# Optimization experiments

Hardware: AMD Instinct MI355X
Metric: run time of the kernel (lower is better)

## Reference

```python
import jax, jax.numpy as jnp
import numpy as np

POS_HALF = 4   # positive window: [t-4, t+4)
NEG_LEN = 12   # negatives: up to 12 frames on each side of the positive window
K_MAX = 2 * POS_HALF + 2 * NEG_LEN  # 32 candidates max per timestep


def _build_windows(T):
    """Static [T,K_MAX] gather indices + positive/valid masks (numpy, trace-time)."""
    idx = np.zeros((T, K_MAX), np.int32)
    pos_mask = np.zeros((T, K_MAX), bool)
    valid = np.zeros((T, K_MAX), bool)
    for t in range(T):
        start, end = max(0, t - POS_HALF), min(T, t + POS_HALF)
        pos = list(range(start, end))
        neg = list(range(max(0, start - NEG_LEN), start)) + \
              list(range(end, min(T, end + NEG_LEN)))
        comb = pos + neg
        idx[t, :len(comb)] = comb
        valid[t, :len(comb)] = True
        pos_mask[t, :len(pos)] = True
    return jnp.asarray(idx), jnp.asarray(pos_mask), jnp.asarray(valid)


def _directional(q, kv, idx, pos_mask, valid, scale, bias):
    # q, kv: [B,T,D] (L2-normalized); idx/pos_mask/valid: [T,K]
    w = kv[:, idx]  # [B,T,K,D] windowed gather
    logits = jnp.einsum('btd,btkd->btk', q, w) * scale + bias  # [B,T,K]
    sign = jnp.where(pos_mask, 1.0, -1.0)
    loglik = jax.nn.log_sigmoid(sign * logits)
    # per-t: sum over window, mean over batch; then sum over t
    loss = -jnp.where(valid, loglik, 0.0).sum(axis=2).mean(axis=0).sum()
    am = jnp.argmax(jnp.where(valid, logits, -jnp.inf), axis=2)  # [B,T]
    T = q.shape[1]
    correct = pos_mask[jnp.arange(T)[None, :], am].astype(jnp.float32).sum()
    return loss, correct


def setup_inputs() -> dict:
    key = jax.random.key(0)
    k1, k2 = jax.random.split(key)
    B, T, D = 8, 1024, 512
    return {
        "motion_feature": jax.random.normal(k1, (B, T, D), jnp.float32),
        "audio_feature": jax.random.normal(k2, (B, T, D), jnp.float32),
        "logit_scale": jnp.asarray(np.log(1.0 / 0.07), jnp.float32),  # param (pre-exp)
        "logit_bias": jnp.asarray(0.0, jnp.float32),                  # param
    }


def reference(motion_feature, audio_feature, logit_scale, logit_bias):
    B, T, _ = motion_feature.shape
    eps = 1e-12
    m = motion_feature / jnp.clip(
        jnp.linalg.norm(motion_feature, axis=2, keepdims=True), eps)
    a = audio_feature / jnp.clip(
        jnp.linalg.norm(audio_feature, axis=2, keepdims=True), eps)
    scale = jnp.exp(logit_scale)
    idx, pos_mask, valid = _build_windows(T)
    m2a_loss, m2a_correct = _directional(m, a, idx, pos_mask, valid, scale, logit_bias)
    a2m_loss, a2m_correct = _directional(a, m, idx, pos_mask, valid, scale, logit_bias)
    final_loss = (m2a_loss + a2m_loss) / (2 * T)
    total_correct = (m2a_correct + a2m_correct) / (2 * T * B)
    return final_loss, total_correct
```

## Files before the change

kernel.cpp:

```cpp
#include <hip/hip_runtime.h>
#include <math.h>

#define B_DIM 8
#define T_DIM 1024
#define D_DIM 512
#define BT (B_DIM * T_DIM)
#define NTILE 64
#define NBLK (B_DIM * NTILE)

typedef __bf16 bf16x8 __attribute__((ext_vector_type(8)));
typedef float floatx4 __attribute__((ext_vector_type(4)));

__device__ __forceinline__ float wave_reduce_sum(float v) {
#pragma unroll
    for (int off = 32; off > 0; off >>= 1) v += __shfl_xor(v, off, 64);
    return v;
}

__device__ __forceinline__ ushort f2bf(float x) {
    unsigned u = __float_as_uint(x);
    return (ushort)((u + 0x7fffu + ((u >> 16) & 1u)) >> 16);
}

__device__ __forceinline__ float softplus(float y) {
    return fmaxf(y, 0.0f) + log1pf(expf(-fabsf(y)));
}

__device__ __forceinline__ bf16x8 load_frag(const float* __restrict__ p) {
    float4 x = *(const float4*)p;
    float4 y = *(const float4*)(p + 4);
    union { ushort u[8]; bf16x8 v; } r;
    r.u[0] = f2bf(x.x); r.u[1] = f2bf(x.y); r.u[2] = f2bf(x.z); r.u[3] = f2bf(x.w);
    r.u[4] = f2bf(y.x); r.u[5] = f2bf(y.y); r.u[6] = f2bf(y.z); r.u[7] = f2bf(y.w);
    return r.v;
}

__global__ __launch_bounds__(256) void norm_kernel(
    const float* __restrict__ m, const float* __restrict__ a,
    float* __restrict__ invm, float* __restrict__ inva)
{
    int wid  = blockIdx.x * 4 + (threadIdx.x >> 6);
    int lane = threadIdx.x & 63;
    const float4* mr = (const float4*)(m + (size_t)wid * D_DIM);
    const float4* ar = (const float4*)(a + (size_t)wid * D_DIM);
    float4 m0 = mr[lane], m1 = mr[lane + 64];
    float4 a0 = ar[lane], a1 = ar[lane + 64];
    float sm = m0.x*m0.x + m0.y*m0.y + m0.z*m0.z + m0.w*m0.w
             + m1.x*m1.x + m1.y*m1.y + m1.z*m1.z + m1.w*m1.w;
    float sa = a0.x*a0.x + a0.y*a0.y + a0.z*a0.z + a0.w*a0.w
             + a1.x*a1.x + a1.y*a1.y + a1.z*a1.z + a1.w*a1.w;
    sm = wave_reduce_sum(sm);
    sa = wave_reduce_sum(sa);
    if (lane == 0) {
        invm[wid] = 1.0f / fmaxf(sqrtf(sm), 1e-12f);
        inva[wid] = 1.0f / fmaxf(sqrtf(sa), 1e-12f);
    }
}

__global__ __launch_bounds__(256) void bandloss_kernel(
    const float* __restrict__ m, const float* __restrict__ a,
    const float* __restrict__ invm, const float* __restrict__ inva,
    const float* __restrict__ pscale, const float* __restrict__ pbias,
    float2* __restrict__ pm,
    float* __restrict__ part_loss, float* __restrict__ part_corr)
{
    __shared__ float red[4][3][256];
    __shared__ float Sbuf[16][48];
    __shared__ float rowpos[16];
    __shared__ float shl[4];

    int blk = blockIdx.x;
    int b   = blk >> 6;
    int t0  = (blk & 63) << 4;
    int tid  = threadIdx.x;
    int w    = tid >> 6;
    int lane = tid & 63;
    int mrow = lane & 15;
    int kgrp = lane >> 4;

    const float* mb = m + ((size_t)b << 19);
    const float* ab = a + ((size_t)b << 19);
    int koff = w * 128 + kgrp * 8;

    const float* arow = mb + (size_t)(t0 + mrow) * D_DIM + koff;
    int j0 = max(t0 - 16 + mrow, 0);
    int j1 = t0 + mrow;
    int j2 = min(t0 + 16 + mrow, T_DIM - 1);
    const float* br0 = ab + (size_t)j0 * D_DIM + koff;
    const float* br1 = ab + (size_t)j1 * D_DIM + koff;
    const float* br2 = ab + (size_t)j2 * D_DIM + koff;

    floatx4 acc0 = {0,0,0,0}, acc1 = {0,0,0,0}, acc2 = {0,0,0,0};
#pragma unroll
    for (int ks = 0; ks < 4; ++ks) {
        bf16x8 af = load_frag(arow + ks * 32);
        bf16x8 f0 = load_frag(br0 + ks * 32);
        bf16x8 f1 = load_frag(br1 + ks * 32);
        bf16x8 f2 = load_frag(br2 + ks * 32);
        acc0 = __builtin_amdgcn_mfma_f32_16x16x32_bf16(af, f0, acc0, 0, 0, 0);
        acc1 = __builtin_amdgcn_mfma_f32_16x16x32_bf16(af, f1, acc1, 0, 0, 0);
        acc2 = __builtin_amdgcn_mfma_f32_16x16x32_bf16(af, f2, acc2, 0, 0, 0);
    }

#pragma unroll
    for (int r = 0; r < 4; ++r) {
        int rr = (kgrp * 4 + r) * 16 + mrow;
        red[w][0][rr] = acc0[r];
        red[w][1][rr] = acc1[r];
        red[w][2][rr] = acc2[r];
    }
    __syncthreads();

    int i  = tid >> 4;
    int cc = tid & 15;
    float s[3];
#pragma unroll
    for (int jt = 0; jt < 3; ++jt)
        s[jt] = red[0][jt][tid] + red[1][jt][tid]
              + red[2][jt][tid] + red[3][jt][tid];
#pragma unroll
    for (int jt = 0; jt < 3; ++jt)
        Sbuf[i][jt * 16 + cc] = s[jt];

    float scale = expf(pscale[0]), bias = pbias[0];
    float im_i  = invm[(b << 10) + t0 + i];
    float loss = 0.0f;
    float mmax = -1e30f, mpos = 0.0f;
#pragma unroll
    for (int jt = 0; jt < 3; ++jt) {
        int k  = jt * 16 + cc;
        int dd = k - i;
        int c  = t0 - 16 + k;
        bool cv = (c >= 0) && (c < T_DIM);
        if (cv && dd >= 0 && dd <= 32) {
            float ia_c  = inva[(b << 10) + c];
            float sv    = s[jt] * ia_c;
            float logit = sv * im_i * scale + bias;
            if (dd < 32) {
                bool pos = (dd >= 12) && (dd <= 19);
                loss += softplus(pos ? -logit : logit);
                if (sv > mmax) { mmax = sv; mpos = pos ? 1.0f : 0.0f; }
            }
            if (dd > 0) {
                bool pos = (dd >= 13) && (dd <= 20);
                loss += softplus(pos ? -logit : logit);
            }
        }
    }

#pragma unroll
    for (int off = 1; off < 16; off <<= 1) {
        float ov = __shfl_xor(mmax, off, 64);
        float op = __shfl_xor(mpos, off, 64);
        if (ov > mmax) { mmax = ov; mpos = op; }
    }
    if (cc == 0) rowpos[i] = mpos;

    loss = wave_reduce_sum(loss);
    if (lane == 0) shl[w] = loss;
    __syncthreads();

    if (tid < 48) {
        int k = tid;
        int c = t0 - 16 + k;
        float bv = -1e30f, bp = 0.0f;
        if (c >= 0 && c < T_DIM) {
            int ilo = max(0, k - 32), ihi = min(16, k);
            for (int ii = ilo; ii < ihi; ++ii) {
                float v = Sbuf[ii][k] * invm[(b << 10) + t0 + ii];
                if (v > bv) {
                    bv = v;
                    int dd = k - ii;
                    bp = (dd >= 13 && dd <= 20) ? 1.0f : 0.0f;
                }
            }
        }
        pm[blk * 48 + k] = make_float2(bv, bp);
    }
    if (tid == 0) {
        float cs = 0.0f;
        for (int r = 0; r < 16; ++r) cs += rowpos[r];
        part_loss[blk] = shl[0] + shl[1] + shl[2] + shl[3];
        part_corr[blk] = cs;
    }
}

__global__ __launch_bounds__(1024) void final2_kernel(
    const float2* __restrict__ pm,
    const float* __restrict__ part_loss, const float* __restrict__ part_corr,
    float* __restrict__ out)
{
    int tid = threadIdx.x;
    float corr = 0.0f, loss = 0.0f;

    for (int x = tid; x < BT; x += 1024) {
        int b = x >> 10, c = x & 1023;
        int tc = c >> 4;
        float bv = -1e30f, bp = 0.0f;
#pragma unroll
        for (int dp = -1; dp <= 1; ++dp) {
            int p = tc + dp;
            if (p < 0 || p >= NTILE) continue;
            int k = c - (p << 4) + 16;
            float2 v = pm[((b << 6) + p) * 48 + k];
            if (v.x > bv) { bv = v.x; bp = v.y; }
        }
        corr += bp;
    }
    if (tid < NBLK) {
        loss = part_loss[tid];
        corr += part_corr[tid];
    }

    loss = wave_reduce_sum(loss);
    corr = wave_reduce_sum(corr);
    __shared__ float shl[16], shc[16];
    int wv = tid >> 6, lane = tid & 63;
    if (lane == 0) { shl[wv] = loss; shc[wv] = corr; }
    __syncthreads();
    if (tid == 0) {
        float L = 0.0f, C = 0.0f;
#pragma unroll
        for (int r = 0; r < 16; ++r) { L += shl[r]; C += shc[r]; }
        out[0] = L / 16384.0f;
        out[1] = C / 16384.0f;
    }
}

extern "C" void kernel_launch(void* const* d_in, const int* in_sizes, int n_in,
                              void* d_out, int out_size, void* d_ws, size_t ws_size,
                              hipStream_t stream)
{
    const float* m  = (const float*)d_in[0];
    const float* a  = (const float*)d_in[1];
    const float* ps = (const float*)d_in[2];
    const float* pb = (const float*)d_in[3];
    float* out = (float*)d_out;

    float*  ws        = (float*)d_ws;
    float*  invm      = ws;
    float*  inva      = ws + BT;
    float2* pm        = (float2*)(ws + 2 * BT);
    float*  part_loss = (float*)(pm + NBLK * 48);
    float*  part_corr = part_loss + NBLK;

    norm_kernel<<<BT / 4, 256, 0, stream>>>(m, a, invm, inva);
    bandloss_kernel<<<NBLK, 256, 0, stream>>>(m, a, invm, inva, ps, pb,
                                              pm, part_loss, part_corr);
    final2_kernel<<<1, 1024, 0, stream>>>(pm, part_loss, part_corr, out);
}
```

Measured before the change: 102.9 us.

## Fuse normalization into band kernel and compute both directions per tile

Drops the separate norm kernel by accumulating squared norms inside the band kernel while loading fragments. Each block now loads three 16-row tiles of both motion and audio and computes a 3x3 grid of MFMA tiles. This lets it evaluate the m2a and a2m rows locally, with argmax per row and per column, and removes the cross-tile partial-max buffer and gather pass in the final kernel. The cost is redundant loads of neighbouring rows, because each block reads 48 rows of both inputs, plus more MFMAs and shared memory per block, in exchange for two fewer launches-worth of work and no norm round trip.

```diff
diff --git a/kernel.cpp b/kernel.cpp
--- a/kernel.cpp
+++ b/kernel.cpp
@@ -1,12 +1,12 @@
 #include <hip/hip_runtime.h>
+#include <hip/hip_bf16.h>
 #include <math.h>
 
 #define B_DIM 8
 #define T_DIM 1024
 #define D_DIM 512
 #define BT (B_DIM * T_DIM)
-#define NTILE 64
-#define NBLK (B_DIM * NTILE)
+#define NBLK 512
 
 typedef __bf16 bf16x8 __attribute__((ext_vector_type(8)));
 typedef float floatx4 __attribute__((ext_vector_type(4)));
@@ -17,57 +17,33 @@
     return v;
 }
 
-__device__ __forceinline__ ushort f2bf(float x) {
-    unsigned u = __float_as_uint(x);
-    return (ushort)((u + 0x7fffu + ((u >> 16) & 1u)) >> 16);
-}
-
 __device__ __forceinline__ float softplus(float y) {
     return fmaxf(y, 0.0f) + log1pf(expf(-fabsf(y)));
 }
 
-__device__ __forceinline__ bf16x8 load_frag(const float* __restrict__ p) {
-    float4 x = *(const float4*)p;
-    float4 y = *(const float4*)(p + 4);
+__device__ __forceinline__ bf16x8 cvt8(float4 x, float4 y) {
     union { ushort u[8]; bf16x8 v; } r;
-    r.u[0] = f2bf(x.x); r.u[1] = f2bf(x.y); r.u[2] = f2bf(x.z); r.u[3] = f2bf(x.w);
-    r.u[4] = f2bf(y.x); r.u[5] = f2bf(y.y); r.u[6] = f2bf(y.z); r.u[7] = f2bf(y.w);
+    __hip_bfloat162 h0 = __float22bfloat162_rn(make_float2(x.x, x.y));
+    __hip_bfloat162 h1 = __float22bfloat162_rn(make_float2(x.z, x.w));
+    __hip_bfloat162 h2 = __float22bfloat162_rn(make_float2(y.x, y.y));
+    __hip_bfloat162 h3 = __float22bfloat162_rn(make_float2(y.z, y.w));
+    ushort2 p0 = *(ushort2*)&h0, p1 = *(ushort2*)&h1;
+    ushort2 p2 = *(ushort2*)&h2, p3 = *(ushort2*)&h3;
+    r.u[0] = p0.x; r.u[1] = p0.y; r.u[2] = p1.x; r.u[3] = p1.y;
+    r.u[4] = p2.x; r.u[5] = p2.y; r.u[6] = p3.x; r.u[7] = p3.y;
     return r.v;
 }
 
-__global__ __launch_bounds__(256) void norm_kernel(
+__global__ __launch_bounds__(256, 2) void bigband_kernel(
     const float* __restrict__ m, const float* __restrict__ a,
-    float* __restrict__ invm, float* __restrict__ inva)
-{
-    int wid  = blockIdx.x * 4 + (threadIdx.x >> 6);
-    int lane = threadIdx.x & 63;
-    const float4* mr = (const float4*)(m + (size_t)wid * D_DIM);
-    const float4* ar = (const float4*)(a + (size_t)wid * D_DIM);
-    float4 m0 = mr[lane], m1 = mr[lane + 64];
-    float4 a0 = ar[lane], a1 = ar[lane + 64];
-    float sm = m0.x*m0.x + m0.y*m0.y + m0.z*m0.z + m0.w*m0.w
-             + m1.x*m1.x + m1.y*m1.y + m1.z*m1.z + m1.w*m1.w;
-    float sa = a0.x*a0.x + a0.y*a0.y + a0.z*a0.z + a0.w*a0.w
-             + a1.x*a1.x + a1.y*a1.y + a1.z*a1.z + a1.w*a1.w;
-    sm = wave_reduce_sum(sm);
-    sa = wave_reduce_sum(sa);
-    if (lane == 0) {
-        invm[wid] = 1.0f / fmaxf(sqrtf(sm), 1e-12f);
-        inva[wid] = 1.0f / fmaxf(sqrtf(sa), 1e-12f);
-    }
-}
-
-__global__ __launch_bounds__(256) void bandloss_kernel(
-    const float* __restrict__ m, const float* __restrict__ a,
-    const float* __restrict__ invm, const float* __restrict__ inva,
     const float* __restrict__ pscale, const float* __restrict__ pbias,
-    float2* __restrict__ pm,
     float* __restrict__ part_loss, float* __restrict__ part_corr)
 {
-    __shared__ float red[4][3][256];
-    __shared__ float Sbuf[16][48];
-    __shared__ float rowpos[16];
-    __shared__ float shl[4];
+    __shared__ float red[4][9][272];
+    __shared__ float Sbuf[48][49];
+    __shared__ float red2[4][6][16];
+    __shared__ float norms[6][16];
+    __shared__ float rowpos[16], colpos[16], shl[4];
 
     int blk = blockIdx.x;
     int b   = blk >> 6;
@@ -77,153 +53,175 @@
     int lane = tid & 63;
     int mrow = lane & 15;
     int kgrp = lane >> 4;
+    int koff = w * 128 + kgrp * 8;
 
     const float* mb = m + ((size_t)b << 19);
     const float* ab = a + ((size_t)b << 19);
-    int koff = w * 128 + kgrp * 8;
-
-    const float* arow = mb + (size_t)(t0 + mrow) * D_DIM + koff;
-    int j0 = max(t0 - 16 + mrow, 0);
-    int j1 = t0 + mrow;
-    int j2 = min(t0 + 16 + mrow, T_DIM - 1);
-    const float* br0 = ab + (size_t)j0 * D_DIM + koff;
-    const float* br1 = ab + (size_t)j1 * D_DIM + koff;
-    const float* br2 = ab + (size_t)j2 * D_DIM + koff;
-
-    floatx4 acc0 = {0,0,0,0}, acc1 = {0,0,0,0}, acc2 = {0,0,0,0};
+
+    const float* mp[3]; const float* ap[3];
+#pragma unroll
+    for (int s = 0; s < 3; ++s) {
+        int r = t0 - 16 + s * 16 + mrow;
+        r = min(max(r, 0), T_DIM - 1);
+        mp[s] = mb + (size_t)r * D_DIM + koff;
+        ap[s] = ab + (size_t)r * D_DIM + koff;
+    }
+
+    floatx4 acc[3][3];
+#pragma unroll
+    for (int ti = 0; ti < 3; ++ti)
+#pragma unroll
+        for (int tj = 0; tj < 3; ++tj) acc[ti][tj] = (floatx4){0.f,0.f,0.f,0.f};
+    float ssm[3] = {0.f,0.f,0.f}, ssa[3] = {0.f,0.f,0.f};
+
 #pragma unroll
     for (int ks = 0; ks < 4; ++ks) {
-        bf16x8 af = load_frag(arow + ks * 32);
-        bf16x8 f0 = load_frag(br0 + ks * 32);
-        bf16x8 f1 = load_frag(br1 + ks * 32);
-        bf16x8 f2 = load_frag(br2 + ks * 32);
-        acc0 = __builtin_amdgcn_mfma_f32_16x16x32_bf16(af, f0, acc0, 0, 0, 0);
-        acc1 = __builtin_amdgcn_mfma_f32_16x16x32_bf16(af, f1, acc1, 0, 0, 0);
-        acc2 = __builtin_amdgcn_mfma_f32_16x16x32_bf16(af, f2, acc2, 0, 0, 0);
-    }
-
-#pragma unroll
-    for (int r = 0; r < 4; ++r) {
-        int rr = (kgrp * 4 + r) * 16 + mrow;
-        red[w][0][rr] = acc0[r];
-        red[w][1][rr] = acc1[r];
-        red[w][2][rr] = acc2[r];
-    }
-    __syncthreads();
-
-    int i  = tid >> 4;
-    int cc = tid & 15;
-    float s[3];
-#pragma unroll
-    for (int jt = 0; jt < 3; ++jt)
-        s[jt] = red[0][jt][tid] + red[1][jt][tid]
-              + red[2][jt][tid] + red[3][jt][tid];
-#pragma unroll
-    for (int jt = 0; jt < 3; ++jt)
-        Sbuf[i][jt * 16 + cc] = s[jt];
+        bf16x8 am[3], av[3];
+#pragma unroll
+        for (int s = 0; s < 3; ++s) {
+            float4 x = *(const float4*)(mp[s] + ks * 32);
+            float4 y = *(const float4*)(mp[s] + ks * 32 + 4);
+            ssm[s] += x.x*x.x + x.y*x.y + x.z*x.z + x.w*x.w
+                    + y.x*y.x + y.y*y.y + y.z*y.z + y.w*y.w;
+            am[s] = cvt8(x, y);
+            float4 u = *(const float4*)(ap[s] + ks * 32);
+            float4 v = *(const float4*)(ap[s] + ks * 32 + 4);
+            ssa[s] += u.x*u.x + u.y*u.y + u.z*u.z + u.w*u.w
+                    + v.x*v.x + v.y*v.y + v.z*v.z + v.w*v.w;
+            av[s] = cvt8(u, v);
+        }
+#pragma unroll
+        for (int ti = 0; ti < 3; ++ti)
+#pragma unroll
+            for (int tj = 0; tj < 3; ++tj)
+                acc[ti][tj] = __builtin_amdgcn_mfma_f32_16x16x32_bf16(
+                    am[ti], av[tj], acc[ti][tj], 0, 0, 0);
+    }
+
+#pragma unroll
+    for (int off = 16; off <= 32; off <<= 1) {
+#pragma unroll
+        for (int s = 0; s < 3; ++s) {
+            ssm[s] += __shfl_xor(ssm[s], off, 64);
+            ssa[s] += __shfl_xor(ssa[s], off, 64);
+        }
+    }
+    if (kgrp == 0) {
+#pragma unroll
+        for (int s = 0; s < 3; ++s) {
+            red2[w][s][mrow]     = ssm[s];
+            red2[w][3 + s][mrow] = ssa[s];
+        }
+    }
+#pragma unroll
+    for (int ti = 0; ti < 3; ++ti)
+#pragma unroll
+        for (int tj = 0; tj < 3; ++tj)
+#pragma unroll
+            for (int r = 0; r < 4; ++r)
+                red[w][ti * 3 + tj][(kgrp * 4 + r) * 17 + mrow] = acc[ti][tj][r];
+    __syncthreads();
+
+    if (tid < 96) {
+        int slot = tid >> 4, mr = tid & 15;
+        float ss = red2[0][slot][mr] + red2[1][slot][mr]
+                 + red2[2][slot][mr] + red2[3][slot][mr];
+        norms[slot][mr] = 1.0f / fmaxf(sqrtf(ss), 1e-12f);
+    }
+    int rho = tid >> 4, kap = tid & 15;
+#pragma unroll
+    for (int ti = 0; ti < 3; ++ti)
+#pragma unroll
+        for (int tj = 0; tj < 3; ++tj) {
+            int tt = ti * 3 + tj;
+            float s4 = red[0][tt][rho * 17 + kap] + red[1][tt][rho * 17 + kap]
+                     + red[2][tt][rho * 17 + kap] + red[3][tt][rho * 17 + kap];
+            Sbuf[ti * 16 + rho][tj * 16 + kap] = s4;
+        }
+    __syncthreads();
 
     float scale = expf(pscale[0]), bias = pbias[0];
-    float im_i  = invm[(b << 10) + t0 + i];
+    int i = rho, cc = kap;
     float loss = 0.0f;
-    float mmax = -1e30f, mpos = 0.0f;
-#pragma unroll
-    for (int jt = 0; jt < 3; ++jt) {
-        int k  = jt * 16 + cc;
-        int dd = k - i;
-        int c  = t0 - 16 + k;
-        bool cv = (c >= 0) && (c < T_DIM);
-        if (cv && dd >= 0 && dd <= 32) {
-            float ia_c  = inva[(b << 10) + c];
-            float sv    = s[jt] * ia_c;
-            float logit = sv * im_i * scale + bias;
-            if (dd < 32) {
+
+    {
+        float im_u = norms[1][i];
+        float mmax = -1e30f, mpos = 0.0f;
+#pragma unroll
+        for (int tj = 0; tj < 3; ++tj) {
+            int v  = tj * 16 + cc;
+            int dd = v - i;
+            int c  = t0 - 16 + v;
+            if (dd >= 0 && dd < 32 && c >= 0 && c < T_DIM) {
+                float sv = Sbuf[16 + i][v] * norms[3 + tj][cc];
+                float logit = sv * im_u * scale + bias;
                 bool pos = (dd >= 12) && (dd <= 19);
                 loss += softplus(pos ? -logit : logit);
                 if (sv > mmax) { mmax = sv; mpos = pos ? 1.0f : 0.0f; }
             }
-            if (dd > 0) {
-                bool pos = (dd >= 13) && (dd <= 20);
+        }
+#pragma unroll
+        for (int off = 1; off < 16; off <<= 1) {
+            float ov = __shfl_xor(mmax, off, 64);
+            float op = __shfl_xor(mpos, off, 64);
+            if (ov > mmax) { mmax = ov; mpos = op; }
+        }
+        if (cc == 0) rowpos[i] = mpos;
+    }
+
+    {
+        float ia_v = norms[4][i];
+        float amax = -1e30f, apos = 0.0f;
+#pragma unroll
+        for (int tj = 0; tj < 3; ++tj) {
+            int u2 = tj * 16 + cc;
+            int ee = u2 - i;
+            int r  = t0 - 16 + u2;
+            if (ee >= 0 && ee < 32 && r >= 0 && r < T_DIM) {
+                float sv = Sbuf[u2][16 + i] * norms[tj][cc];
+                float logit = sv * ia_v * scale + bias;
+                bool pos = (ee >= 12) && (ee <= 19);
                 loss += softplus(pos ? -logit : logit);
+                if (sv > amax) { amax = sv; apos = pos ? 1.0f : 0.0f; }
             }
         }
-    }
-
-#pragma unroll
-    for (int off = 1; off < 16; off <<= 1) {
-        float ov = __shfl_xor(mmax, off, 64);
-        float op = __shfl_xor(mpos, off, 64);
-        if (ov > mmax) { mmax = ov; mpos = op; }
-    }
-    if (cc == 0) rowpos[i] = mpos;
+#pragma unroll
+        for (int off = 1; off < 16; off <<= 1) {
+            float ov = __shfl_xor(amax, off, 64);
+            float op = __shfl_xor(apos, off, 64);
+            if (ov > amax) { amax = ov; apos = op; }
+        }
+        if (cc == 0) colpos[i] = apos;
+    }
 
     loss = wave_reduce_sum(loss);
     if (lane == 0) shl[w] = loss;
     __syncthreads();
-
-    if (tid < 48) {
-        int k = tid;
-        int c = t0 - 16 + k;
-        float bv = -1e30f, bp = 0.0f;
-        if (c >= 0 && c < T_DIM) {
-            int ilo = max(0, k - 32), ihi = min(16, k);
-            for (int ii = ilo; ii < ihi; ++ii) {
-                float v = Sbuf[ii][k] * invm[(b << 10) + t0 + ii];
-                if (v > bv) {
-                    bv = v;
-                    int dd = k - ii;
-                    bp = (dd >= 13 && dd <= 20) ? 1.0f : 0.0f;
-                }
-            }
-        }
-        pm[blk * 48 + k] = make_float2(bv, bp);
-    }
     if (tid == 0) {
-        float cs = 0.0f;
-        for (int r = 0; r < 16; ++r) cs += rowpos[r];
+        float C = 0.0f;
+#pragma unroll
+        for (int r = 0; r < 16; ++r) C += rowpos[r] + colpos[r];
         part_loss[blk] = shl[0] + shl[1] + shl[2] + shl[3];
-        part_corr[blk] = cs;
-    }
-}
-
-__global__ __launch_bounds__(1024) void final2_kernel(
-    const float2* __restrict__ pm,
+        part_corr[blk] = C;
+    }
+}
+
+__global__ __launch_bounds__(256) void finalsum_kernel(
     const float* __restrict__ part_loss, const float* __restrict__ part_corr,
     float* __restrict__ out)
 {
     int tid = threadIdx.x;
-    float corr = 0.0f, loss = 0.0f;
-
-    for (int x = tid; x < BT; x += 1024) {
-        int b = x >> 10, c = x & 1023;
-        int tc = c >> 4;
-        float bv = -1e30f, bp = 0.0f;
-#pragma unroll
-        for (int dp = -1; dp <= 1; ++dp) {
-            int p = tc + dp;
-            if (p < 0 || p >= NTILE) continue;
-            int k = c - (p << 4) + 16;
-            float2 v = pm[((b << 6) + p) * 48 + k];
-            if (v.x > bv) { bv = v.x; bp = v.y; }
-        }
-        corr += bp;
-    }
-    if (tid < NBLK) {
-        loss = part_loss[tid];
-        corr += part_corr[tid];
-    }
-
-    loss = wave_reduce_sum(loss);
-    corr = wave_reduce_sum(corr);
-    __shared__ float shl[16], shc[16];
-    int wv = tid >> 6, lane = tid & 63;
-    if (lane == 0) { shl[wv] = loss; shc[wv] = corr; }
+    float l = part_loss[tid] + part_loss[tid + 256];
+    float c = part_corr[tid] + part_corr[tid + 256];
+    l = wave_reduce_sum(l);
+    c = wave_reduce_sum(c);
+    __shared__ float shl[4], shc[4];
+    int w = tid >> 6, lane = tid & 63;
+    if (lane == 0) { shl[w] = l; shc[w] = c; }
     __syncthreads();
     if (tid == 0) {
-        float L = 0.0f, C = 0.0f;
-#pragma unroll
-        for (int r = 0; r < 16; ++r) { L += shl[r]; C += shc[r]; }
-        out[0] = L / 16384.0f;
-        out[1] = C / 16384.0f;
+        out[0] = (shl[0] + shl[1] + shl[2] + shl[3]) / 16384.0f;
+        out[1] = (shc[0] + shc[1] + shc[2] + shc[3]) / 16384.0f;
     }
 }
 
@@ -237,15 +235,9 @@
     const float* pb = (const float*)d_in[3];
     float* out = (float*)d_out;
 
-    float*  ws        = (float*)d_ws;
-    float*  invm      = ws;
-    float*  inva      = ws + BT;
-    float2* pm        = (float2*)(ws + 2 * BT);
-    float*  part_loss = (float*)(pm + NBLK * 48);
-    float*  part_corr = part_loss + NBLK;
-
-    norm_kernel<<<BT / 4, 256, 0, stream>>>(m, a, invm, inva);
-    bandloss_kernel<<<NBLK, 256, 0, stream>>>(m, a, invm, inva, ps, pb,
-                                              pm, part_loss, part_corr);
-    final2_kernel<<<1, 1024, 0, stream>>>(pm, part_loss, part_corr, out);
-}
+    float* part_loss = (float*)d_ws;
+    float* part_corr = part_loss + NBLK;
+
+    bigband_kernel<<<NBLK, 256, 0, stream>>>(m, a, ps, pb, part_loss, part_corr);
+    finalsum_kernel<<<1, 256, 0, stream>>>(part_loss, part_corr, out);
+}
```

After: 93.05 us. -9.6%, faster.

## Fuse L2 norm computation into band-loss kernel and drop separate norm pass

Applied to the files above, without the earlier changes.

Computes per-row sum of squares for motion and the three audio row bands inside the band-loss kernel from the same float4 loads used for the MFMA fragments, reducing across waves in shared memory, and removes the standalone norm kernel and its workspace. This avoids a full extra read of both inputs and one kernel launch. It also switches bf16 conversion to the HIP packed intrinsic and pads shared reduction arrays to cut bank conflicts. Adds an extra block barrier and some redundant sum-of-squares work on overlapping audio rows across blocks.

```diff
diff --git a/kernel.cpp b/kernel.cpp
--- a/kernel.cpp
+++ b/kernel.cpp
@@ -1,4 +1,5 @@
 #include <hip/hip_runtime.h>
+#include <hip/hip_bf16.h>
 #include <math.h>
 
 #define B_DIM 8
@@ -17,57 +18,34 @@
     return v;
 }
 
-__device__ __forceinline__ ushort f2bf(float x) {
-    unsigned u = __float_as_uint(x);
-    return (ushort)((u + 0x7fffu + ((u >> 16) & 1u)) >> 16);
-}
-
 __device__ __forceinline__ float softplus(float y) {
     return fmaxf(y, 0.0f) + log1pf(expf(-fabsf(y)));
 }
 
-__device__ __forceinline__ bf16x8 load_frag(const float* __restrict__ p) {
-    float4 x = *(const float4*)p;
-    float4 y = *(const float4*)(p + 4);
+__device__ __forceinline__ bf16x8 cvt8(float4 x, float4 y) {
     union { ushort u[8]; bf16x8 v; } r;
-    r.u[0] = f2bf(x.x); r.u[1] = f2bf(x.y); r.u[2] = f2bf(x.z); r.u[3] = f2bf(x.w);
-    r.u[4] = f2bf(y.x); r.u[5] = f2bf(y.y); r.u[6] = f2bf(y.z); r.u[7] = f2bf(y.w);
+    __hip_bfloat162 h0 = __float22bfloat162_rn(make_float2(x.x, x.y));
+    __hip_bfloat162 h1 = __float22bfloat162_rn(make_float2(x.z, x.w));
+    __hip_bfloat162 h2 = __float22bfloat162_rn(make_float2(y.x, y.y));
+    __hip_bfloat162 h3 = __float22bfloat162_rn(make_float2(y.z, y.w));
+    ushort2 p0 = *(ushort2*)&h0, p1 = *(ushort2*)&h1;
+    ushort2 p2 = *(ushort2*)&h2, p3 = *(ushort2*)&h3;
+    r.u[0] = p0.x; r.u[1] = p0.y; r.u[2] = p1.x; r.u[3] = p1.y;
+    r.u[4] = p2.x; r.u[5] = p2.y; r.u[6] = p3.x; r.u[7] = p3.y;
     return r.v;
-}
-
-__global__ __launch_bounds__(256) void norm_kernel(
-    const float* __restrict__ m, const float* __restrict__ a,
-    float* __restrict__ invm, float* __restrict__ inva)
-{
-    int wid  = blockIdx.x * 4 + (threadIdx.x >> 6);
-    int lane = threadIdx.x & 63;
-    const float4* mr = (const float4*)(m + (size_t)wid * D_DIM);
-    const float4* ar = (const float4*)(a + (size_t)wid * D_DIM);
-    float4 m0 = mr[lane], m1 = mr[lane + 64];
-    float4 a0 = ar[lane], a1 = ar[lane + 64];
-    float sm = m0.x*m0.x + m0.y*m0.y + m0.z*m0.z + m0.w*m0.w
-             + m1.x*m1.x + m1.y*m1.y + m1.z*m1.z + m1.w*m1.w;
-    float sa = a0.x*a0.x + a0.y*a0.y + a0.z*a0.z + a0.w*a0.w
-             + a1.x*a1.x + a1.y*a1.y + a1.z*a1.z + a1.w*a1.w;
-    sm = wave_reduce_sum(sm);
-    sa = wave_reduce_sum(sa);
-    if (lane == 0) {
-        invm[wid] = 1.0f / fmaxf(sqrtf(sm), 1e-12f);
-        inva[wid] = 1.0f / fmaxf(sqrtf(sa), 1e-12f);
-    }
 }
 
 __global__ __launch_bounds__(256) void bandloss_kernel(
     const float* __restrict__ m, const float* __restrict__ a,
-    const float* __restrict__ invm, const float* __restrict__ inva,
     const float* __restrict__ pscale, const float* __restrict__ pbias,
     float2* __restrict__ pm,
     float* __restrict__ part_loss, float* __restrict__ part_corr)
 {
-    __shared__ float red[4][3][256];
-    __shared__ float Sbuf[16][48];
-    __shared__ float rowpos[16];
-    __shared__ float shl[4];
+    __shared__ float red[4][3][272];
+    __shared__ float red2[4][4][16];
+    __shared__ float norms[4][16];
+    __shared__ float Sbuf[16][49];
+    __shared__ float rowpos[16], shl[4];
 
     int blk = blockIdx.x;
     int b   = blk >> 6;
@@ -77,53 +55,79 @@
     int lane = tid & 63;
     int mrow = lane & 15;
     int kgrp = lane >> 4;
+    int koff = w * 128 + kgrp * 8;
 
     const float* mb = m + ((size_t)b << 19);
     const float* ab = a + ((size_t)b << 19);
-    int koff = w * 128 + kgrp * 8;
-
-    const float* arow = mb + (size_t)(t0 + mrow) * D_DIM + koff;
-    int j0 = max(t0 - 16 + mrow, 0);
-    int j1 = t0 + mrow;
-    int j2 = min(t0 + 16 + mrow, T_DIM - 1);
-    const float* br0 = ab + (size_t)j0 * D_DIM + koff;
-    const float* br1 = ab + (size_t)j1 * D_DIM + koff;
-    const float* br2 = ab + (size_t)j2 * D_DIM + koff;
-
-    floatx4 acc0 = {0,0,0,0}, acc1 = {0,0,0,0}, acc2 = {0,0,0,0};
+
+    const float* mp = mb + (size_t)(t0 + mrow) * D_DIM + koff;
+    const float* ap[3];
+#pragma unroll
+    for (int s = 0; s < 3; ++s) {
+        int r = t0 - 16 + s * 16 + mrow;
+        r = min(max(r, 0), T_DIM - 1);
+        ap[s] = ab + (size_t)r * D_DIM + koff;
+    }
+
+    floatx4 acc[3] = {{0,0,0,0},{0,0,0,0},{0,0,0,0}};
+    float ssm = 0.f, ssa[3] = {0.f,0.f,0.f};
+
 #pragma unroll
     for (int ks = 0; ks < 4; ++ks) {
-        bf16x8 af = load_frag(arow + ks * 32);
-        bf16x8 f0 = load_frag(br0 + ks * 32);
-        bf16x8 f1 = load_frag(br1 + ks * 32);
-        bf16x8 f2 = load_frag(br2 + ks * 32);
-        acc0 = __builtin_amdgcn_mfma_f32_16x16x32_bf16(af, f0, acc0, 0, 0, 0);
-        acc1 = __builtin_amdgcn_mfma_f32_16x16x32_bf16(af, f1, acc1, 0, 0, 0);
-        acc2 = __builtin_amdgcn_mfma_f32_16x16x32_bf16(af, f2, acc2, 0, 0, 0);
-    }
-
-#pragma unroll
-    for (int r = 0; r < 4; ++r) {
-        int rr = (kgrp * 4 + r) * 16 + mrow;
-        red[w][0][rr] = acc0[r];
-        red[w][1][rr] = acc1[r];
-        red[w][2][rr] = acc2[r];
-    }
-    __syncthreads();
-
+        float4 x = *(const float4*)(mp + ks * 32);
+        float4 y = *(const float4*)(mp + ks * 32 + 4);
+        ssm += x.x*x.x + x.y*x.y + x.z*x.z + x.w*x.w
+             + y.x*y.x + y.y*y.y + y.z*y.z + y.w*y.w;
+        bf16x8 am = cvt8(x, y);
+#pragma unroll
+        for (int s = 0; s < 3; ++s) {
+            float4 u = *(const float4*)(ap[s] + ks * 32);
+            float4 v = *(const float4*)(ap[s] + ks * 32 + 4);
+            ssa[s] += u.x*u.x + u.y*u.y + u.z*u.z + u.w*u.w
+                    + v.x*v.x + v.y*v.y + v.z*v.z + v.w*v.w;
+            acc[s] = __builtin_amdgcn_mfma_f32_16x16x32_bf16(
+                am, cvt8(u, v), acc[s], 0, 0, 0);
+        }
+    }
+
+#pragma unroll
+    for (int off = 16; off <= 32; off <<= 1) {
+        ssm += __shfl_xor(ssm, off, 64);
+#pragma unroll
+        for (int s = 0; s < 3; ++s) ssa[s] += __shfl_xor(ssa[s], off, 64);
+    }
+    if (kgrp == 0) {
+        red2[w][0][mrow] = ssm;
+#pragma unroll
+        for (int s = 0; s < 3; ++s) red2[w][1 + s][mrow] = ssa[s];
+    }
+#pragma unroll
+    for (int s = 0; s < 3; ++s)
+#pragma unroll
+        for (int r = 0; r < 4; ++r)
+            red[w][s][(kgrp * 4 + r) * 17 + mrow] = acc[s][r];
+    __syncthreads();
+
+    if (tid < 64) {
+        int slot = tid >> 4, mr = tid & 15;
+        float ss = red2[0][slot][mr] + red2[1][slot][mr]
+                 + red2[2][slot][mr] + red2[3][slot][mr];
+        norms[slot][mr] = 1.0f / fmaxf(sqrtf(ss), 1e-12f);
+    }
     int i  = tid >> 4;
     int cc = tid & 15;
     float s[3];
 #pragma unroll
     for (int jt = 0; jt < 3; ++jt)
-        s[jt] = red[0][jt][tid] + red[1][jt][tid]
-              + red[2][jt][tid] + red[3][jt][tid];
+        s[jt] = red[0][jt][i * 17 + cc] + red[1][jt][i * 17 + cc]
+              + red[2][jt][i * 17 + cc] + red[3][jt][i * 17 + cc];
 #pragma unroll
     for (int jt = 0; jt < 3; ++jt)
         Sbuf[i][jt * 16 + cc] = s[jt];
+    __syncthreads();
 
     float scale = expf(pscale[0]), bias = pbias[0];
-    float im_i  = invm[(b << 10) + t0 + i];
+    float im_i  = norms[0][i];
     float loss = 0.0f;
     float mmax = -1e30f, mpos = 0.0f;
 #pragma unroll
@@ -133,7 +137,7 @@
         int c  = t0 - 16 + k;
         bool cv = (c >= 0) && (c < T_DIM);
         if (cv && dd >= 0 && dd <= 32) {
-            float ia_c  = inva[(b << 10) + c];
+            float ia_c  = norms[1 + jt][cc];
             float sv    = s[jt] * ia_c;
             float logit = sv * im_i * scale + bias;
             if (dd < 32) {
@@ -167,7 +171,7 @@
         if (c >= 0 && c < T_DIM) {
             int ilo = max(0, k - 32), ihi = min(16, k);
             for (int ii = ilo; ii < ihi; ++ii) {
-                float v = Sbuf[ii][k] * invm[(b << 10) + t0 + ii];
+                float v = Sbuf[ii][k] * norms[0][ii];
                 if (v > bv) {
                     bv = v;
                     int dd = k - ii;
@@ -237,15 +241,11 @@
     const float* pb = (const float*)d_in[3];
     float* out = (float*)d_out;
 
-    float*  ws        = (float*)d_ws;
-    float*  invm      = ws;
-    float*  inva      = ws + BT;
-    float2* pm        = (float2*)(ws + 2 * BT);
+    float2* pm        = (float2*)d_ws;
     float*  part_loss = (float*)(pm + NBLK * 48);
     float*  part_corr = part_loss + NBLK;
 
-    norm_kernel<<<BT / 4, 256, 0, stream>>>(m, a, invm, inva);
-    bandloss_kernel<<<NBLK, 256, 0, stream>>>(m, a, invm, inva, ps, pb,
+    bandloss_kernel<<<NBLK, 256, 0, stream>>>(m, a, ps, pb,
                                               pm, part_loss, part_corr);
     final2_kernel<<<1, 1024, 0, stream>>>(pm, part_loss, part_corr, out);
 }
```

New measurement: 97.15 us. 5.6% less time.
